# Kernel tuning notes

Measured on AMD Instinct MI355X. Metric: run time of the kernel, lower is better.

Reference implementation:

```python
import jax, jax.numpy as jnp
import numpy as np

B, S, I, H, C = 512, 128, 64, 256, 10


def setup_inputs() -> dict:
    key = jax.random.key(0)
    ks = jax.random.split(key, 9)
    u = lambda k, shape, lo, hi: jax.random.uniform(k, shape, jnp.float32, lo, hi)
    return {
        "x": jax.random.normal(ks[0], (B, S, I), jnp.float32),
        # LTCCell params (uniform init per init_parameters)
        "W_gd": u(ks[1], (2 * H, I + H), -0.1, 0.1),
        "b_gd": u(ks[2], (2 * H,), -0.1, 0.1),
        "W_tau": u(ks[3], (H, H), -0.1, 0.1),
        "b_tau": u(ks[4], (H,), -0.1, 0.1),
        "gleak": u(ks[5], (H,), 0.001, 1.0),
        "cm": u(ks[6], (H,), 0.4, 0.6),
        # classifier head
        "W_fc": jax.random.normal(ks[7], (C, H), jnp.float32) * 0.05,
        "b_fc": jax.random.normal(ks[8], (C,), jnp.float32) * 0.05,
    }


def reference(x, W_gd, b_gd, W_tau, b_tau, gleak, cm, W_fc, b_fc):
    # Constant part of the denominator (elementwise, hidden_dim)
    const_den = jax.nn.softplus(cm) + jax.nn.softplus(gleak)  # [H]

    def dhdt(h, x_t):
        # LTCCell.forward: dh/dt
        combined = jnp.concatenate([x_t, h], axis=1)          # [B, I+H]
        gd = combined @ W_gd.T + b_gd                          # [B, 2H]
        gate, dyn = jnp.split(gd, 2, axis=1)
        tau = jax.nn.softplus(h @ W_tau.T + b_tau)             # [B, H]
        num = jax.nn.sigmoid(gate) * jnp.tanh(dyn) - h
        return num / (tau + const_den + 1e-6)

    def step(h, x_t):
        # torchdiffeq 'rk4' fixed-grid = 3/8-rule RK4, single step dt=1 over [0,1]
        k1 = dhdt(h, x_t)
        k2 = dhdt(h + k1 / 3.0, x_t)
        k3 = dhdt(h + (k2 - k1 / 3.0), x_t)
        k4 = dhdt(h + (k1 - k2 + k3), x_t)
        h_new = h + (k1 + 3.0 * (k2 + k3) + k4) * 0.125
        return h_new, None

    h0 = jnp.zeros((x.shape[0], H), x.dtype)
    xs = jnp.transpose(x, (1, 0, 2))                           # [S, B, I]
    h_final, _ = jax.lax.scan(step, h0, xs)
    return h_final @ W_fc.T + b_fc                             # [B, C]
```

## Files before the change

kernel.cpp:

```cpp
#include <hip/hip_runtime.h>

typedef __attribute__((ext_vector_type(8))) short bf16x8;
typedef __attribute__((ext_vector_type(4))) float f32x4;
typedef __attribute__((ext_vector_type(2))) _Float16 f16x2;

#define MFMA(a, b, c) __builtin_amdgcn_mfma_f32_16x16x32_bf16((a), (b), (c), 0, 0, 0)

__device__ __forceinline__ unsigned short f2bf(float f) {
    unsigned int u = __builtin_bit_cast(unsigned int, f);
    return (unsigned short)((u + 0x7FFFu + ((u >> 16) & 1u)) >> 16);
}
__device__ __forceinline__ float softplusf(float v) {
    return __logf(1.f + __expf(v));
}

__global__ __launch_bounds__(256) void prepack_kernel(const float* __restrict__ W_gd,
                                                      unsigned short* __restrict__ ws) {
    int i = blockIdx.x * 256 + threadIdx.x;
    ws[i] = f2bf(W_gd[(256 + (i >> 8)) * 320 + 64 + (i & 255)]);
    if (i < 32768) ws[65536 + i] = f2bf(W_gd[(i >> 6) * 320 + (i & 63)]);
}

__global__ __launch_bounds__(512, 1)
void ltc_kernel(
    const float* __restrict__ x, const float* __restrict__ W_gd,
    const float* __restrict__ b_gd, const float* __restrict__ W_tau,
    const float* __restrict__ b_tau, const float* __restrict__ gleak,
    const float* __restrict__ cm, const float* __restrict__ W_fc,
    const float* __restrict__ b_fc, const unsigned short* __restrict__ ws,
    float* __restrict__ out)
{
    const int tid  = threadIdx.x;
    const int lane = tid & 63;
    const int wv   = tid >> 6;
    const int c16  = lane & 15;
    const int kg   = lane >> 4;
    const int kg8  = kg * 8;
    const int row0 = blockIdx.x * 2;

    __shared__ __align__(16) unsigned short tauL[65536];
    __shared__ __align__(16) unsigned short dynL[4096];
    __shared__ __align__(16) unsigned short abuf[2][2][264];
    __shared__ __align__(16) unsigned short xbuf[2][72];
    __shared__ __align__(8)  float tcL[512];
    __shared__ float bgdL[512];
    __shared__ float hout[2][257];

    for (int i = tid; i < 65536; i += 512) {
        int u = i >> 8, k = i & 255;
        tauL[u * 256 + (k ^ ((u & 15) << 3))] = f2bf(W_tau[i]);
    }
    for (int i = tid; i < 4096; i += 512) {
        int uidx = i >> 5, k = i & 31;
        int u = (uidx >> 4) * 32 + (uidx & 15);
        dynL[uidx * 32 + (k ^ ((uidx & 3) << 3))] = f2bf(W_gd[(256 + u) * 320 + 64 + k]);
    }
    for (int i = tid; i < 2 * 2 * 264; i += 512) ((unsigned short*)abuf)[i] = 0;
    if (tid < 256) {
        tcL[2 * tid]     = b_tau[tid];
        tcL[2 * tid + 1] = softplusf(cm[tid]) + softplusf(gleak[tid]) + 1e-6f;
    }
    bgdL[tid] = b_gd[tid];

    const int uA = 32 * wv + c16;
    const int uB = uA + 16;
    const int tswz = c16 << 3;
    const unsigned short* tAb = tauL + uA * 256;
    const unsigned short* tBb = tauL + uB * 256;
    const bf16x8* dA0p = (const bf16x8*)(dynL + (wv * 16 + c16) * 32 + (kg8 ^ ((c16 & 3) << 3)));
    const int vOffA = uA * 256 + kg8;
    const int vOffB = vOffA + 16 * 256;
    const int vOffX = 65536 + uA * 64 + kg8;

    bf16x8 Wg[2][8];
    {
        const int wrow[2] = { uA, uB };
        #pragma unroll
        for (int t = 0; t < 2; ++t) {
            const float* src = W_gd + wrow[t] * 320 + 64;
            #pragma unroll
            for (int s = 0; s < 8; ++s) {
                const float4* p = (const float4*)(src + s * 32 + kg8);
                float4 a = p[0], b = p[1];
                bf16x8 v;
                v[0] = (short)f2bf(a.x); v[1] = (short)f2bf(a.y);
                v[2] = (short)f2bf(a.z); v[3] = (short)f2bf(a.w);
                v[4] = (short)f2bf(b.x); v[5] = (short)f2bf(b.y);
                v[6] = (short)f2bf(b.z); v[7] = (short)f2bf(b.w);
                Wg[t][s] = v;
            }
        }
    }

    const int rsel = (c16 < 2) ? c16 : 0;
    const unsigned short* aptrP0 = &abuf[0][rsel][kg8];
    const unsigned short* aptrP1 = &abuf[1][rsel][kg8];
    const unsigned short* xptr   = &xbuf[rsel][kg8];

    float hv[2][2] = {{0.f, 0.f}, {0.f, 0.f}};
    f16x2 zh; zh[0] = (_Float16)0.f; zh[1] = (_Float16)0.f;
    f16x2 kk1[2] = { zh, zh }, kk2[2] = { zh, zh }, kk3[2] = { zh, zh };

    bf16x8 pipe[5];
    #pragma unroll
    for (int i = 0; i < 5; ++i)
        pipe[i] = *(const bf16x8*)(ws + vOffA + (i + 1) * 32);

    __syncthreads();

#define ELEM(ti, G, D, den, en)                                                  \
    _Pragma("unroll")                                                            \
    for (int r = 0; r < 2; ++r) {                                                \
        float gate = G[r] + (float)gdx[ti][r];                                   \
        float dyn  = D[r] + (float)gdx[2 + ti][r];                               \
        float sig = __fdividef(1.f, 1.f + __expf(-gate));                        \
        float th  = 1.f - __fdividef(2.f, __expf(2.f * dyn) + 1.f);              \
        float k1v = (float)kk1[ti][r], k2v = (float)kk2[ti][r], k3v = (float)kk3[ti][r]; \
        float h0 = hv[ti][r];                                                    \
        float ec;                                                                \
        if      (stg == 0) ec = h0;                                              \
        else if (stg == 1) ec = h0 + k1v * (1.f / 3.f);                          \
        else if (stg == 2) ec = h0 - k1v * (1.f / 3.f) + k2v;                    \
        else               ec = h0 + k1v - k2v + k3v;                            \
        float kv = __fdividef(sig * th - ec, den[r]);                            \
        if (stg == 0)      { kk1[ti][r] = (_Float16)kv; en[r] = h0 + kv * (1.f / 3.f); } \
        else if (stg == 1) { kk2[ti][r] = (_Float16)kv; en[r] = h0 - k1v * (1.f / 3.f) + kv; } \
        else if (stg == 2) { kk3[ti][r] = (_Float16)kv; en[r] = h0 + k1v - k2v + kv; } \
        else               { en[r] = h0 + 0.125f * (k1v + 3.f * (k2v + k3v) + kv); hv[ti][r] = en[r]; } \
    }

    #pragma unroll 1
    for (int ts = 0; ts < 128; ++ts) {
        if (tid < 128) {
            int r = tid >> 6, i = tid & 63;
            xbuf[r][i] = f2bf(x[((row0 + r) * 128 + ts) * 64 + i]);
        }
        __syncthreads();

        f32x4 gx0 = {0,0,0,0}, gx1 = {0,0,0,0}, gx2 = {0,0,0,0}, gx3 = {0,0,0,0};
        #pragma unroll
        for (int s = 0; s < 2; ++s) {
            bf16x8 ax = *(const bf16x8*)(xptr + s * 32);
            gx0 = MFMA(ax, *(const bf16x8*)(ws + vOffX + s * 32), gx0);
            gx1 = MFMA(ax, *(const bf16x8*)(ws + vOffX + 16 * 64 + s * 32), gx1);
            gx2 = MFMA(ax, *(const bf16x8*)(ws + vOffX + 256 * 64 + s * 32), gx2);
            gx3 = MFMA(ax, *(const bf16x8*)(ws + vOffX + 272 * 64 + s * 32), gx3);
        }
        f16x2 gdx[4];
        {
            float bg0 = bgdL[uA], bg1 = bgdL[uB], bg2 = bgdL[256 + uA], bg3 = bgdL[256 + uB];
            gdx[0][0] = (_Float16)(gx0[0] + bg0); gdx[0][1] = (_Float16)(gx0[1] + bg0);
            gdx[1][0] = (_Float16)(gx1[0] + bg1); gdx[1][1] = (_Float16)(gx1[1] + bg1);
            gdx[2][0] = (_Float16)(gx2[0] + bg2); gdx[2][1] = (_Float16)(gx2[1] + bg2);
            gdx[3][0] = (_Float16)(gx3[0] + bg3); gdx[3][1] = (_Float16)(gx3[1] + bg3);
        }

        #pragma unroll
        for (int stg = 0; stg < 4; ++stg) {
            const unsigned short* aptr = (stg & 1) ? aptrP1 : aptrP0;
            unsigned short (*wbuf)[264] = abuf[(stg & 1) ^ 1];

            f32x4 T0 = {0,0,0,0}, G0 = {0,0,0,0}, D0 = {0,0,0,0};
            {
                bf16x8 A = *(const bf16x8*)(aptr);
                T0 = MFMA(A, *(const bf16x8*)(tAb + (kg8 ^ tswz)), T0);
                G0 = MFMA(A, Wg[0][0], G0);
                D0 = MFMA(A, *dA0p, D0);
            }
            #pragma unroll
            for (int s = 1; s < 8; ++s) {
                bf16x8 A = *(const bf16x8*)(aptr + s * 32);
                T0 = MFMA(A, *(const bf16x8*)(tAb + ((s * 32 + kg8) ^ tswz)), T0);
                G0 = MFMA(A, Wg[0][s], G0);
                D0 = MFMA(A, pipe[(s - 1) % 5], D0);
                if (s <= 2) pipe[(s - 1) % 5] = *(const bf16x8*)(ws + vOffA + (s + 5) * 32);
                else        pipe[(s - 1) % 5] = *(const bf16x8*)(ws + vOffB + (s - 3) * 32);
            }
            float2 tc0 = *(const float2*)(tcL + 2 * uA);
            float den0[2];
            den0[0] = softplusf(T0[0] + tc0.x) + tc0.y;
            den0[1] = softplusf(T0[1] + tc0.x) + tc0.y;
            float en0[2];
            ELEM(0, G0, D0, den0, en0);
            if (lane < 16) { wbuf[0][uA] = f2bf(en0[0]); wbuf[1][uA] = f2bf(en0[1]); }

            f32x4 T1 = {0,0,0,0}, G1 = {0,0,0,0}, D1 = {0,0,0,0};
            #pragma unroll
            for (int s = 0; s < 8; ++s) {
                bf16x8 A = *(const bf16x8*)(aptr + s * 32);
                T1 = MFMA(A, *(const bf16x8*)(tBb + ((s * 32 + kg8) ^ tswz)), T1);
                G1 = MFMA(A, Wg[1][s], G1);
                D1 = MFMA(A, pipe[(7 + s) % 5], D1);
                if (s <= 2) pipe[(7 + s) % 5] = *(const bf16x8*)(ws + vOffB + (5 + s) * 32);
                else        pipe[(7 + s) % 5] = *(const bf16x8*)(ws + vOffA + (s - 2) * 32);
            }
            float2 tc1 = *(const float2*)(tcL + 2 * uB);
            float den1[2];
            den1[0] = softplusf(T1[0] + tc1.x) + tc1.y;
            den1[1] = softplusf(T1[1] + tc1.x) + tc1.y;
            float en1[2];
            ELEM(1, G1, D1, den1, en1);
            if (lane < 16) { wbuf[0][uB] = f2bf(en1[0]); wbuf[1][uB] = f2bf(en1[1]); }

            __syncthreads();
        }
    }
#undef ELEM

    if (lane < 16) {
        hout[0][uA] = hv[0][0]; hout[1][uA] = hv[0][1];
        hout[0][uB] = hv[1][0]; hout[1][uB] = hv[1][1];
    }
    __syncthreads();
    if (tid < 20) {
        int r = tid / 10, c = tid % 10;
        float acc = b_fc[c];
        for (int k = 0; k < 256; ++k) acc = fmaf(hout[r][k], W_fc[c * 256 + k], acc);
        out[(row0 + r) * 10 + c] = acc;
    }
}

extern "C" void kernel_launch(void* const* d_in, const int* in_sizes, int n_in,
                              void* d_out, int out_size, void* d_ws, size_t ws_size,
                              hipStream_t stream) {
    (void)in_sizes; (void)n_in; (void)out_size; (void)ws_size;
    unsigned short* ws16 = (unsigned short*)d_ws;
    prepack_kernel<<<256, 256, 0, stream>>>((const float*)d_in[1], ws16);
    ltc_kernel<<<256, 512, 0, stream>>>(
        (const float*)d_in[0], (const float*)d_in[1], (const float*)d_in[2],
        (const float*)d_in[3], (const float*)d_in[4], (const float*)d_in[5],
        (const float*)d_in[6], (const float*)d_in[7], (const float*)d_in[8],
        ws16, (float*)d_out);
}
```

Measured before the change: 1.013 ms.

## Hold W_tau and W_gd gate weights in AGPRs via inline MFMA asm

Drops the 128KB LDS copy of W_tau and instead keeps each wave's W_tau rows, like the W_gd gate rows, in registers. Inline asm MFMAs take those weights from accumulation registers, and manual s_nop padding covers MFMA hazards. The A operand is loaded once per stage and reused for both unit halves, and the dyn-weight prefetch pipe grows from 5 to 10 entries with a new rotation. This removes the per-stage LDS reads of W_tau, at the cost of much higher register pressure, hand-written hazard nops, and fragile pipe indexing.

```diff
diff --git a/kernel.cpp b/kernel.cpp
--- a/kernel.cpp
+++ b/kernel.cpp
@@ -5,6 +5,8 @@
 typedef __attribute__((ext_vector_type(2))) _Float16 f16x2;
 
 #define MFMA(a, b, c) __builtin_amdgcn_mfma_f32_16x16x32_bf16((a), (b), (c), 0, 0, 0)
+#define MFMA_AG(acc, va, ab) \
+    asm("s_nop 1\n\tv_mfma_f32_16x16x32_bf16 %0, %1, %2, %0" : "+v"(acc) : "v"(va), "a"(ab))
 
 __device__ __forceinline__ unsigned short f2bf(float f) {
     unsigned int u = __builtin_bit_cast(unsigned int, f);
@@ -38,7 +40,6 @@
     const int kg8  = kg * 8;
     const int row0 = blockIdx.x * 2;
 
-    __shared__ __align__(16) unsigned short tauL[65536];
     __shared__ __align__(16) unsigned short dynL[4096];
     __shared__ __align__(16) unsigned short abuf[2][2][264];
     __shared__ __align__(16) unsigned short xbuf[2][72];
@@ -46,10 +47,6 @@
     __shared__ float bgdL[512];
     __shared__ float hout[2][257];
 
-    for (int i = tid; i < 65536; i += 512) {
-        int u = i >> 8, k = i & 255;
-        tauL[u * 256 + (k ^ ((u & 15) << 3))] = f2bf(W_tau[i]);
-    }
     for (int i = tid; i < 4096; i += 512) {
         int uidx = i >> 5, k = i & 31;
         int u = (uidx >> 4) * 32 + (uidx & 15);
@@ -64,30 +61,35 @@
 
     const int uA = 32 * wv + c16;
     const int uB = uA + 16;
-    const int tswz = c16 << 3;
-    const unsigned short* tAb = tauL + uA * 256;
-    const unsigned short* tBb = tauL + uB * 256;
     const bf16x8* dA0p = (const bf16x8*)(dynL + (wv * 16 + c16) * 32 + (kg8 ^ ((c16 & 3) << 3)));
     const int vOffA = uA * 256 + kg8;
     const int vOffB = vOffA + 16 * 256;
     const int vOffX = 65536 + uA * 64 + kg8;
 
-    bf16x8 Wg[2][8];
+    bf16x8 Wg[2][8], Wt[2][8];
     {
         const int wrow[2] = { uA, uB };
         #pragma unroll
         for (int t = 0; t < 2; ++t) {
-            const float* src = W_gd + wrow[t] * 320 + 64;
+            const float* gsrc = W_gd + wrow[t] * 320 + 64;
+            const float* tsrc = W_tau + wrow[t] * 256;
             #pragma unroll
             for (int s = 0; s < 8; ++s) {
-                const float4* p = (const float4*)(src + s * 32 + kg8);
-                float4 a = p[0], b = p[1];
+                const float4* gp = (const float4*)(gsrc + s * 32 + kg8);
+                const float4* tp = (const float4*)(tsrc + s * 32 + kg8);
+                float4 a = gp[0], b = gp[1];
                 bf16x8 v;
                 v[0] = (short)f2bf(a.x); v[1] = (short)f2bf(a.y);
                 v[2] = (short)f2bf(a.z); v[3] = (short)f2bf(a.w);
                 v[4] = (short)f2bf(b.x); v[5] = (short)f2bf(b.y);
                 v[6] = (short)f2bf(b.z); v[7] = (short)f2bf(b.w);
                 Wg[t][s] = v;
+                a = tp[0]; b = tp[1];
+                v[0] = (short)f2bf(a.x); v[1] = (short)f2bf(a.y);
+                v[2] = (short)f2bf(a.z); v[3] = (short)f2bf(a.w);
+                v[4] = (short)f2bf(b.x); v[5] = (short)f2bf(b.y);
+                v[6] = (short)f2bf(b.z); v[7] = (short)f2bf(b.w);
+                Wt[t][s] = v;
             }
         }
     }
@@ -101,10 +103,13 @@
     f16x2 zh; zh[0] = (_Float16)0.f; zh[1] = (_Float16)0.f;
     f16x2 kk1[2] = { zh, zh }, kk2[2] = { zh, zh }, kk3[2] = { zh, zh };
 
-    bf16x8 pipe[5];
+    bf16x8 pipe[10];
     #pragma unroll
-    for (int i = 0; i < 5; ++i)
+    for (int i = 0; i < 7; ++i)
         pipe[i] = *(const bf16x8*)(ws + vOffA + (i + 1) * 32);
+    #pragma unroll
+    for (int i = 0; i < 3; ++i)
+        pipe[7 + i] = *(const bf16x8*)(ws + vOffB + i * 32);
 
     __syncthreads();
 
@@ -157,25 +162,27 @@
 
         #pragma unroll
         for (int stg = 0; stg < 4; ++stg) {
-            const unsigned short* aptr = (stg & 1) ? aptrP1 : aptrP0;
-            unsigned short (*wbuf)[264] = abuf[(stg & 1) ^ 1];
+            const int p = stg & 1;
+            const unsigned short* aptr = p ? aptrP1 : aptrP0;
+            unsigned short (*wbuf)[264] = abuf[p ^ 1];
+
+            bf16x8 Af[8];
+            #pragma unroll
+            for (int s = 0; s < 8; ++s) Af[s] = *(const bf16x8*)(aptr + s * 32);
 
             f32x4 T0 = {0,0,0,0}, G0 = {0,0,0,0}, D0 = {0,0,0,0};
-            {
-                bf16x8 A = *(const bf16x8*)(aptr);
-                T0 = MFMA(A, *(const bf16x8*)(tAb + (kg8 ^ tswz)), T0);
-                G0 = MFMA(A, Wg[0][0], G0);
-                D0 = MFMA(A, *dA0p, D0);
+            MFMA_AG(T0, Af[0], Wt[0][0]);
+            MFMA_AG(G0, Af[0], Wg[0][0]);
+            D0 = MFMA(Af[0], *dA0p, D0);
+            #pragma unroll
+            for (int s = 1; s < 8; ++s) {
+                MFMA_AG(T0, Af[s], Wt[0][s]);
+                MFMA_AG(G0, Af[s], Wg[0][s]);
+                D0 = MFMA(Af[s], pipe[(s - 1 + 5 * p) % 10], D0);
+                if (s <= 5) pipe[(s - 1 + 5 * p) % 10] = *(const bf16x8*)(ws + vOffB + (s + 2) * 32);
+                else        pipe[(s - 1 + 5 * p) % 10] = *(const bf16x8*)(ws + vOffA + (s - 5) * 32);
             }
-            #pragma unroll
-            for (int s = 1; s < 8; ++s) {
-                bf16x8 A = *(const bf16x8*)(aptr + s * 32);
-                T0 = MFMA(A, *(const bf16x8*)(tAb + ((s * 32 + kg8) ^ tswz)), T0);
-                G0 = MFMA(A, Wg[0][s], G0);
-                D0 = MFMA(A, pipe[(s - 1) % 5], D0);
-                if (s <= 2) pipe[(s - 1) % 5] = *(const bf16x8*)(ws + vOffA + (s + 5) * 32);
-                else        pipe[(s - 1) % 5] = *(const bf16x8*)(ws + vOffB + (s - 3) * 32);
-            }
+            asm volatile("s_nop 7\n\ts_nop 7\n\ts_nop 7" : "+v"(T0), "+v"(G0));
             float2 tc0 = *(const float2*)(tcL + 2 * uA);
             float den0[2];
             den0[0] = softplusf(T0[0] + tc0.x) + tc0.y;
@@ -187,13 +194,13 @@
             f32x4 T1 = {0,0,0,0}, G1 = {0,0,0,0}, D1 = {0,0,0,0};
             #pragma unroll
             for (int s = 0; s < 8; ++s) {
-                bf16x8 A = *(const bf16x8*)(aptr + s * 32);
-                T1 = MFMA(A, *(const bf16x8*)(tBb + ((s * 32 + kg8) ^ tswz)), T1);
-                G1 = MFMA(A, Wg[1][s], G1);
-                D1 = MFMA(A, pipe[(7 + s) % 5], D1);
-                if (s <= 2) pipe[(7 + s) % 5] = *(const bf16x8*)(ws + vOffB + (5 + s) * 32);
-                else        pipe[(7 + s) % 5] = *(const bf16x8*)(ws + vOffA + (s - 2) * 32);
+                MFMA_AG(T1, Af[s], Wt[1][s]);
+                MFMA_AG(G1, Af[s], Wg[1][s]);
+                D1 = MFMA(Af[s], pipe[(7 + s + 5 * p) % 10], D1);
+                if (s <= 4) pipe[(7 + s + 5 * p) % 10] = *(const bf16x8*)(ws + vOffA + (s + 3) * 32);
+                else        pipe[(7 + s + 5 * p) % 10] = *(const bf16x8*)(ws + vOffB + (s - 5) * 32);
             }
+            asm volatile("s_nop 7\n\ts_nop 7\n\ts_nop 7" : "+v"(T1), "+v"(G1));
             float2 tc1 = *(const float2*)(tcL + 2 * uB);
             float den1[2];
             den1[0] = softplusf(T1[0] + tc1.x) + tc1.y;
```

New measurement: 3.462 ms. +241.6%, slower.
